# Kernel tuning notes

Hardware: AMD Instinct MI355X
Metric: run time of the kernel (lower is better)

The kernel has to match this reference:

```python
import jax, jax.numpy as jnp
import numpy as np

N = 100000
E = 1600000
IN_DIM = 165
HID = 128
OUT_H = 64  # hidden_dim // 2

def setup_inputs() -> dict:
    key = jax.random.key(0)
    ks = jax.random.split(key, 8)
    x = jax.random.normal(ks[0], (N, IN_DIM), dtype=jnp.float32)
    edge_index = jax.random.randint(ks[1], (2, E), 0, N, dtype=jnp.int64)
    s1 = 1.0 / np.sqrt(IN_DIM)
    s2 = 1.0 / np.sqrt(HID)
    s3 = 1.0 / np.sqrt(OUT_H)
    return {
        "x": x,
        "edge_index": edge_index,
        "W1": jax.random.normal(ks[2], (IN_DIM, HID), dtype=jnp.float32) * s1,
        "b1": jnp.zeros((HID,), jnp.float32),
        "Wg": jax.random.normal(ks[3], (HID, OUT_H), dtype=jnp.float32) * s2,
        "a_src": jax.random.normal(ks[4], (OUT_H,), dtype=jnp.float32) * s3,
        "a_dst": jax.random.normal(ks[5], (OUT_H,), dtype=jnp.float32) * s3,
        "bg": jnp.zeros((OUT_H,), jnp.float32),
        "Wfc": jax.random.normal(ks[6], (OUT_H, 2), dtype=jnp.float32) * s3,
        "bfc": jnp.zeros((2,), jnp.float32),
    }

def _add_self_loops(edge_index, n):
    loops = jnp.arange(n, dtype=edge_index.dtype)
    row = jnp.concatenate([edge_index[0], loops])
    col = jnpp_concat = jnp.concatenate([edge_index[1], loops])
    return row, col

def _gcn_layer(x, row, col, W, b, n):
    deg = jax.ops.segment_sum(jnp.ones_like(col, dtype=x.dtype), col, num_segments=n)
    dinv = jnp.where(deg > 0, jax.lax.rsqrt(deg), 0.0)
    h = x @ W                                   # [N, HID]
    msg = h[row] * (dinv[row] * dinv[col])[:, None]  # [E+N, HID]
    return jax.ops.segment_sum(msg, col, num_segments=n) + b

def _gat_layer(x, row, col, W, a_src, a_dst, b, n):
    # single-head GATConv with self-loops, LeakyReLU(0.2), segment softmax over dst
    h = x @ W                                   # [N, OUT_H]
    e = jax.nn.leaky_relu((h @ a_src)[row] + (h @ a_dst)[col], negative_slope=0.2)
    m = jax.ops.segment_max(e, col, num_segments=n)
    ex = jnp.exp(e - m[col])
    s = jax.ops.segment_sum(ex, col, num_segments=n)
    alpha = ex / s[col]                         # every node has a self-loop => s > 0
    out = jax.ops.segment_sum(alpha[:, None] * h[row], col, num_segments=n)
    return out + b

def reference(x, edge_index, W1, b1, Wg, a_src, a_dst, bg, Wfc, bfc):
    n = x.shape[0]
    row, col = _add_self_loops(edge_index, n)
    h = jax.nn.relu(_gcn_layer(x, row, col, W1, b1, n))
    h = jax.nn.relu(_gat_layer(h, row, col, Wg, a_src, a_dst, bg, n))
    return h @ Wfc + bfc
```

## Files before the change

### kernel.cpp

```cpp
#include <hip/hip_runtime.h>
#include <math.h>

#define NSL 0.2f
#define IN_DIM 165
#define HID 128
#define OUT_H 64
#define NCB_MAX 512
#define EPB 4096

typedef __attribute__((ext_vector_type(8))) short bf16x8;
typedef __attribute__((ext_vector_type(4))) float f32x4;

__device__ inline unsigned pack_bf16(float a, float b) {
    unsigned ua = __float_as_uint(a);
    ua += 0x7FFFu + ((ua >> 16) & 1u);
    unsigned ub = __float_as_uint(b);
    ub += 0x7FFFu + ((ub >> 16) & 1u);
    return (ua >> 16) | (ub & 0xFFFF0000u);
}

__device__ __host__ inline int pcol(int i) {
    int j = i >> 1, odd = i & 1;
    return 32 * (j >> 4) + (j & 15) + 16 * odd;
}

__global__ __launch_bounds__(256) void chist(const int* __restrict__ coli, int E,
                                             int* __restrict__ ghist, int ncb) {
    __shared__ int h[NCB_MAX];
    for (int i = threadIdx.x; i < ncb; i += 256) h[i] = 0;
    __syncthreads();
    int e0 = blockIdx.x * EPB;
    int e1 = min(e0 + EPB, E);
    for (int e = e0 + threadIdx.x; e < e1; e += 256)
        atomicAdd(&h[coli[e] >> 8], 1);
    __syncthreads();
    for (int i = threadIdx.x; i < ncb; i += 256)
        if (h[i]) atomicAdd(&ghist[i], h[i]);
}

__global__ __launch_bounds__(NCB_MAX) void cscan(const int* __restrict__ ghist,
                                                 int* __restrict__ cstart,
                                                 int* __restrict__ gcursor,
                                                 int ncb, int E) {
    __shared__ int tmp[NCB_MAX];
    int tid = threadIdx.x;
    int v = (tid < ncb) ? ghist[tid] : 0;
    tmp[tid] = v;
    __syncthreads();
    for (int off = 1; off < NCB_MAX; off <<= 1) {
        int t = (tid >= off) ? tmp[tid - off] : 0;
        __syncthreads();
        tmp[tid] += t;
        __syncthreads();
    }
    if (tid < ncb) {
        int excl = tmp[tid] - v;
        cstart[tid] = excl;
        gcursor[tid] = excl;
    }
    if (tid == ncb - 1) cstart[ncb] = E;
}

__global__ __launch_bounds__(256) void pass1_scatter(const int* __restrict__ rowi,
                                                     const int* __restrict__ coli, int E,
                                                     int* __restrict__ gcursor,
                                                     unsigned* __restrict__ ebuf, int ncb) {
    __shared__ int hist[NCB_MAX];
    __shared__ int base[NCB_MAX];
    int e0 = blockIdx.x * EPB;
    int e1 = min(e0 + EPB, E);
    for (int i = threadIdx.x; i < ncb; i += 256) hist[i] = 0;
    __syncthreads();
    for (int e = e0 + threadIdx.x; e < e1; e += 256)
        atomicAdd(&hist[coli[e] >> 8], 1);
    __syncthreads();
    for (int i = threadIdx.x; i < ncb; i += 256) {
        int h = hist[i];
        base[i] = h ? atomicAdd(&gcursor[i], h) : 0;
        hist[i] = 0;
    }
    __syncthreads();
    for (int e = e0 + threadIdx.x; e < e1; e += 256) {
        int c = coli[e];
        int cb = c >> 8;
        int rank = atomicAdd(&hist[cb], 1);
        ebuf[base[cb] + rank] = ((unsigned)rowi[e] << 8) | (unsigned)(c & 255);
    }
}

__global__ __launch_bounds__(256) void pass2_all(const unsigned* __restrict__ ebuf,
                                                 const int* __restrict__ cstart,
                                                 int* __restrict__ offsets,
                                                 float* __restrict__ dinv,
                                                 int* __restrict__ csr_src,
                                                 int n, int E) {
    __shared__ int cnt[256];
    __shared__ int scan[256];
    __shared__ int offs[256];
    const int tid = threadIdx.x;
    const int cb = blockIdx.x;
    cnt[tid] = 0;
    __syncthreads();
    int s = cstart[cb], e1 = cstart[cb + 1];
    for (int e = s + tid; e < e1; e += 256)
        atomicAdd(&cnt[ebuf[e] & 255u], 1);
    __syncthreads();
    int v = cnt[tid];
    scan[tid] = v;
    __syncthreads();
#pragma unroll
    for (int off = 1; off < 256; off <<= 1) {
        int t = (tid >= off) ? scan[tid - off] : 0;
        __syncthreads();
        scan[tid] += t;
        __syncthreads();
    }
    int off0 = s + scan[tid] - v;
    offs[tid] = off0;
    int node = (cb << 8) + tid;
    if (node < n) {
        offsets[node] = off0;
        dinv[node] = rsqrtf((float)v + 1.0f);
    }
    if (cb == 0 && tid == 0) offsets[n] = E;
    cnt[tid] = 0;
    __syncthreads();
    for (int e = s + tid; e < e1; e += 256) {
        unsigned u = ebuf[e];
        int local = u & 255u;
        int rank = atomicAdd(&cnt[local], 1);
        csr_src[offs[local] + rank] = (int)(u >> 8);
    }
}

__global__ __launch_bounds__(256) void wprep_all(const float* __restrict__ W1,
                                                 const float* __restrict__ b1,
                                                 const float* __restrict__ Wg,
                                                 const float* __restrict__ bg,
                                                 const float* __restrict__ Wfc,
                                                 uint4* __restrict__ wfrag,
                                                 float* __restrict__ b1p,
                                                 uint4* __restrict__ wg2frag,
                                                 float* __restrict__ bgp,
                                                 float2* __restrict__ wfcp) {
    int idx = blockIdx.x * 256 + threadIdx.x;
    if (idx < 3072) {
        int q = idx & 3, n = (idx >> 2) & 127, c = idx >> 9;
        int k0 = c * 32 + q * 8;
        float f[8];
#pragma unroll
        for (int j = 0; j < 8; j++) {
            int k = k0 + j;
            f[j] = (k < IN_DIM) ? W1[k * 128 + n] : 0.f;
        }
        uint4 u;
        u.x = pack_bf16(f[0], f[1]);
        u.y = pack_bf16(f[2], f[3]);
        u.z = pack_bf16(f[4], f[5]);
        u.w = pack_bf16(f[6], f[7]);
        wfrag[idx] = u;
    } else if (idx < 4096) {
        int i2 = idx - 3072;
        int q = i2 & 3, n = (i2 >> 2) & 63, c = i2 >> 8;
        float f[8];
#pragma unroll
        for (int j = 0; j < 8; j++) {
            int ks = c * 32 + q * 8 + j;
            f[j] = Wg[pcol(ks) * 64 + n];
        }
        uint4 u;
        u.x = pack_bf16(f[0], f[1]);
        u.y = pack_bf16(f[2], f[3]);
        u.z = pack_bf16(f[4], f[5]);
        u.w = pack_bf16(f[6], f[7]);
        wg2frag[i2] = u;
    }
    if (idx < 128) b1p[idx] = b1[pcol(idx)];
    if (idx < 64) {
        int o = pcol(idx);
        bgp[idx] = bg[o];
        wfcp[idx] = make_float2(Wfc[o * 2], Wfc[o * 2 + 1]);
    }
}

__global__ __launch_bounds__(256) void gemm1_mfma(const float* __restrict__ x,
                                                  const uint4* __restrict__ wfrag,
                                                  const float* __restrict__ dinv,
                                                  unsigned* __restrict__ h1p, int M) {
    const int t = threadIdx.x;
    const int wave = t >> 6;
    const int lane = t & 63;
    const int l16 = lane & 15;
    const int quad = lane >> 4;
    const int rowbase = blockIdx.x * 64 + wave * 16;

    int arow = rowbase + l16;
    if (arow >= M) arow = M - 1;
    const float* xr = x + (size_t)arow * IN_DIM;

    f32x4 acc[8];
#pragma unroll
    for (int nt = 0; nt < 8; nt++) acc[nt] = (f32x4){0.f, 0.f, 0.f, 0.f};

#pragma unroll
    for (int c = 0; c < 6; c++) {
        int k0 = c * 32 + quad * 8;
        float f[8];
#pragma unroll
        for (int j = 0; j < 8; j++)
            f[j] = (k0 + j < IN_DIM) ? xr[k0 + j] : 0.f;
        uint4 au;
        au.x = pack_bf16(f[0], f[1]);
        au.y = pack_bf16(f[2], f[3]);
        au.z = pack_bf16(f[4], f[5]);
        au.w = pack_bf16(f[6], f[7]);
        bf16x8 a = __builtin_bit_cast(bf16x8, au);
#pragma unroll
        for (int nt = 0; nt < 8; nt++) {
            uint4 bu = wfrag[(size_t)((c * 128 + nt * 16 + l16) * 4 + quad)];
            bf16x8 b = __builtin_bit_cast(bf16x8, bu);
            acc[nt] = __builtin_amdgcn_mfma_f32_16x16x32_bf16(a, b, acc[nt], 0, 0, 0);
        }
    }

#pragma unroll
    for (int r = 0; r < 4; r++) {
        int row = rowbase + quad * 4 + r;
        if (row < M) {
            float s = dinv[row];
#pragma unroll
            for (int p = 0; p < 4; p++) {
                h1p[(size_t)row * 64 + p * 16 + l16] =
                    pack_bf16(acc[2 * p][r] * s, acc[2 * p + 1][r] * s);
            }
        }
    }
}

__device__ inline void acc8(float* a, uint4 u) {
    a[0] += __uint_as_float(u.x << 16);
    a[1] += __uint_as_float(u.x & 0xFFFF0000u);
    a[2] += __uint_as_float(u.y << 16);
    a[3] += __uint_as_float(u.y & 0xFFFF0000u);
    a[4] += __uint_as_float(u.z << 16);
    a[5] += __uint_as_float(u.z & 0xFFFF0000u);
    a[6] += __uint_as_float(u.w << 16);
    a[7] += __uint_as_float(u.w & 0xFFFF0000u);
}

__device__ inline void fma8(float* a, uint4 u, float w) {
    a[0] = fmaf(__uint_as_float(u.x << 16), w, a[0]);
    a[1] = fmaf(__uint_as_float(u.x & 0xFFFF0000u), w, a[1]);
    a[2] = fmaf(__uint_as_float(u.y << 16), w, a[2]);
    a[3] = fmaf(__uint_as_float(u.y & 0xFFFF0000u), w, a[3]);
    a[4] = fmaf(__uint_as_float(u.z << 16), w, a[4]);
    a[5] = fmaf(__uint_as_float(u.z & 0xFFFF0000u), w, a[5]);
    a[6] = fmaf(__uint_as_float(u.w << 16), w, a[6]);
    a[7] = fmaf(__uint_as_float(u.w & 0xFFFF0000u), w, a[7]);
}

__device__ inline float lexp(float e) {
    e = e > 0.f ? e : NSL * e;
    return __expf(e);
}

__global__ __launch_bounds__(256) void gcn_gather(const int* __restrict__ offsets,
                                                  const int* __restrict__ csr_src,
                                                  const uint4* __restrict__ h1v,
                                                  const float* __restrict__ dinv,
                                                  const float* __restrict__ b1p,
                                                  uint4* __restrict__ gb, int n) {
    int node = (blockIdx.x * 256 + threadIdx.x) >> 4;
    int lane = threadIdx.x & 15;
    if (node >= n) return;
    int s0 = offsets[node], s1 = offsets[node + 1];

    float a0[8], a1[8], a2[8], a3[8];
#pragma unroll
    for (int i = 0; i < 8; i++) { a0[i] = 0.f; a1[i] = 0.f; a2[i] = 0.f; a3[i] = 0.f; }
    acc8(a0, h1v[(size_t)node * 16 + lane]);

    int k = s0;
    if (s1 - k >= 4) {
        int r0 = csr_src[k], r1 = csr_src[k + 1], r2 = csr_src[k + 2], r3 = csr_src[k + 3];
        uint4 v0 = h1v[(size_t)r0 * 16 + lane];
        uint4 v1 = h1v[(size_t)r1 * 16 + lane];
        uint4 v2 = h1v[(size_t)r2 * 16 + lane];
        uint4 v3 = h1v[(size_t)r3 * 16 + lane];
        k += 4;
        while (s1 - k >= 4) {
            int q0 = csr_src[k], q1 = csr_src[k + 1], q2 = csr_src[k + 2], q3 = csr_src[k + 3];
            uint4 u0 = h1v[(size_t)q0 * 16 + lane];
            uint4 u1 = h1v[(size_t)q1 * 16 + lane];
            uint4 u2 = h1v[(size_t)q2 * 16 + lane];
            uint4 u3 = h1v[(size_t)q3 * 16 + lane];
            k += 4;
            acc8(a0, v0);
            acc8(a1, v1);
            acc8(a2, v2);
            acc8(a3, v3);
            v0 = u0; v1 = u1; v2 = u2; v3 = u3;
        }
        acc8(a0, v0);
        acc8(a1, v1);
        acc8(a2, v2);
        acc8(a3, v3);
    }
    for (; k < s1; k++) {
        int r = csr_src[k];
        acc8(a0, h1v[(size_t)r * 16 + lane]);
    }

    float dc = dinv[node];
    float4 bb0 = ((const float4*)b1p)[lane * 2];
    float4 bb1 = ((const float4*)b1p)[lane * 2 + 1];
    float o[8];
    o[0] = fmaxf(((a0[0] + a1[0]) + (a2[0] + a3[0])) * dc + bb0.x, 0.f);
    o[1] = fmaxf(((a0[1] + a1[1]) + (a2[1] + a3[1])) * dc + bb0.y, 0.f);
    o[2] = fmaxf(((a0[2] + a1[2]) + (a2[2] + a3[2])) * dc + bb0.z, 0.f);
    o[3] = fmaxf(((a0[3] + a1[3]) + (a2[3] + a3[3])) * dc + bb0.w, 0.f);
    o[4] = fmaxf(((a0[4] + a1[4]) + (a2[4] + a3[4])) * dc + bb1.x, 0.f);
    o[5] = fmaxf(((a0[5] + a1[5]) + (a2[5] + a3[5])) * dc + bb1.y, 0.f);
    o[6] = fmaxf(((a0[6] + a1[6]) + (a2[6] + a3[6])) * dc + bb1.z, 0.f);
    o[7] = fmaxf(((a0[7] + a1[7]) + (a2[7] + a3[7])) * dc + bb1.w, 0.f);
    uint4 pk;
    pk.x = pack_bf16(o[0], o[1]);
    pk.y = pack_bf16(o[2], o[3]);
    pk.z = pack_bf16(o[4], o[5]);
    pk.w = pack_bf16(o[6], o[7]);
    gb[(size_t)node * 16 + lane] = pk;
}

__global__ __launch_bounds__(256) void gemm2_mfma(const uint4* __restrict__ gb4,
                                                  const uint4* __restrict__ wg2frag,
                                                  const float* __restrict__ a_src,
                                                  const float* __restrict__ a_dst,
                                                  unsigned* __restrict__ h2b,
                                                  float* __restrict__ es,
                                                  float* __restrict__ ed, int M) {
    const int t = threadIdx.x;
    const int wave = t >> 6;
    const int lane = t & 63;
    const int l16 = lane & 15;
    const int quad = lane >> 4;
    const int rowbase = blockIdx.x * 64 + wave * 16;

    int arow = rowbase + l16;
    if (arow >= M) arow = M - 1;

    f32x4 acc[4];
#pragma unroll
    for (int nt = 0; nt < 4; nt++) acc[nt] = (f32x4){0.f, 0.f, 0.f, 0.f};

#pragma unroll
    for (int c = 0; c < 4; c++) {
        uint4 au = gb4[(size_t)arow * 16 + c * 4 + quad];
        bf16x8 a = __builtin_bit_cast(bf16x8, au);
#pragma unroll
        for (int nt = 0; nt < 4; nt++) {
            uint4 bu = wg2frag[(size_t)((c * 64 + nt * 16 + l16) * 4 + quad)];
            bf16x8 b = __builtin_bit_cast(bf16x8, bu);
            acc[nt] = __builtin_amdgcn_mfma_f32_16x16x32_bf16(a, b, acc[nt], 0, 0, 0);
        }
    }

    float as0 = a_src[l16], as1 = a_src[16 + l16], as2 = a_src[32 + l16], as3 = a_src[48 + l16];
    float ad0 = a_dst[l16], ad1 = a_dst[16 + l16], ad2 = a_dst[32 + l16], ad3 = a_dst[48 + l16];

#pragma unroll
    for (int r = 0; r < 4; r++) {
        int row = rowbase + quad * 4 + r;
        float ps = acc[0][r] * as0 + acc[1][r] * as1 + acc[2][r] * as2 + acc[3][r] * as3;
        float pd = acc[0][r] * ad0 + acc[1][r] * ad1 + acc[2][r] * ad2 + acc[3][r] * ad3;
#pragma unroll
        for (int m = 8; m; m >>= 1) {
            ps += __shfl_xor(ps, m, 16);
            pd += __shfl_xor(pd, m, 16);
        }
        if (row < M) {
            h2b[(size_t)row * 32 + l16]      = pack_bf16(acc[0][r], acc[1][r]);
            h2b[(size_t)row * 32 + 16 + l16] = pack_bf16(acc[2][r], acc[3][r]);
            if (l16 == 0) { es[row] = ps; ed[row] = pd; }
        }
    }
}

__global__ __launch_bounds__(256) void gat_fused(const int* __restrict__ offsets,
                                                 const int* __restrict__ csr_src,
                                                 const uint4* __restrict__ h2v,
                                                 const float* __restrict__ es,
                                                 const float* __restrict__ ed,
                                                 const float* __restrict__ bgp,
                                                 const float2* __restrict__ wfcp,
                                                 const float* __restrict__ bfc,
                                                 float* __restrict__ out, int n) {
    int node = (blockIdx.x * 256 + threadIdx.x) >> 3;
    int lane = threadIdx.x & 7;
    if (node >= n) return;
    int s0 = offsets[node], s1 = offsets[node + 1];
    float edc = ed[node];

    float x0s = lexp(es[node] + edc);
    float sA = x0s, sB = 0.f, sC = 0.f, sD = 0.f;
    float aA[8], aB[8], aC[8], aD[8];
#pragma unroll
    for (int i = 0; i < 8; i++) { aA[i] = 0.f; aB[i] = 0.f; aC[i] = 0.f; aD[i] = 0.f; }
    fma8(aA, h2v[(size_t)node * 8 + lane], x0s);

    int k = s0;
    if (s1 - k >= 4) {
        int r0 = csr_src[k], r1 = csr_src[k + 1], r2 = csr_src[k + 2], r3 = csr_src[k + 3];
        float e0 = es[r0], e1 = es[r1], e2 = es[r2], e3 = es[r3];
        uint4 v0 = h2v[(size_t)r0 * 8 + lane];
        uint4 v1 = h2v[(size_t)r1 * 8 + lane];
        uint4 v2 = h2v[(size_t)r2 * 8 + lane];
        uint4 v3 = h2v[(size_t)r3 * 8 + lane];
        k += 4;
        while (s1 - k >= 4) {
            int q0 = csr_src[k], q1 = csr_src[k + 1], q2 = csr_src[k + 2], q3 = csr_src[k + 3];
            float f0 = es[q0], f1 = es[q1], f2 = es[q2], f3 = es[q3];
            uint4 u0 = h2v[(size_t)q0 * 8 + lane];
            uint4 u1 = h2v[(size_t)q1 * 8 + lane];
            uint4 u2 = h2v[(size_t)q2 * 8 + lane];
            uint4 u3 = h2v[(size_t)q3 * 8 + lane];
            k += 4;
            float x0 = lexp(e0 + edc), x1 = lexp(e1 + edc);
            float x2 = lexp(e2 + edc), x3 = lexp(e3 + edc);
            sA += x0; sB += x1; sC += x2; sD += x3;
            fma8(aA, v0, x0);
            fma8(aB, v1, x1);
            fma8(aC, v2, x2);
            fma8(aD, v3, x3);
            e0 = f0; e1 = f1; e2 = f2; e3 = f3;
            v0 = u0; v1 = u1; v2 = u2; v3 = u3;
        }
        float x0 = lexp(e0 + edc), x1 = lexp(e1 + edc);
        float x2 = lexp(e2 + edc), x3 = lexp(e3 + edc);
        sA += x0; sB += x1; sC += x2; sD += x3;
        fma8(aA, v0, x0);
        fma8(aB, v1, x1);
        fma8(aC, v2, x2);
        fma8(aD, v3, x3);
    }
    for (; k < s1; k++) {
        int r = csr_src[k];
        float xv = lexp(es[r] + edc);
        sA += xv;
        fma8(aA, h2v[(size_t)r * 8 + lane], xv);
    }
    float s = (sA + sB) + (sC + sD);
    float rcp = 1.0f / s;
    float4 b0 = ((const float4*)bgp)[lane * 2];
    float4 b1 = ((const float4*)bgp)[lane * 2 + 1];
    float o[8];
    o[0] = fmaxf(((aA[0] + aB[0]) + (aC[0] + aD[0])) * rcp + b0.x, 0.f);
    o[1] = fmaxf(((aA[1] + aB[1]) + (aC[1] + aD[1])) * rcp + b0.y, 0.f);
    o[2] = fmaxf(((aA[2] + aB[2]) + (aC[2] + aD[2])) * rcp + b0.z, 0.f);
    o[3] = fmaxf(((aA[3] + aB[3]) + (aC[3] + aD[3])) * rcp + b0.w, 0.f);
    o[4] = fmaxf(((aA[4] + aB[4]) + (aC[4] + aD[4])) * rcp + b1.x, 0.f);
    o[5] = fmaxf(((aA[5] + aB[5]) + (aC[5] + aD[5])) * rcp + b1.y, 0.f);
    o[6] = fmaxf(((aA[6] + aB[6]) + (aC[6] + aD[6])) * rcp + b1.z, 0.f);
    o[7] = fmaxf(((aA[7] + aB[7]) + (aC[7] + aD[7])) * rcp + b1.w, 0.f);

    float p0 = 0.f, p1 = 0.f;
#pragma unroll
    for (int m2 = 0; m2 < 4; m2++) {
        float4 w = ((const float4*)wfcp)[lane * 4 + m2];
        p0 += o[2 * m2] * w.x + o[2 * m2 + 1] * w.z;
        p1 += o[2 * m2] * w.y + o[2 * m2 + 1] * w.w;
    }
#pragma unroll
    for (int m = 4; m; m >>= 1) {
        p0 += __shfl_xor(p0, m, 8);
        p1 += __shfl_xor(p1, m, 8);
    }
    if (lane == 0) {
        out[(size_t)node * 2 + 0] = p0 + bfc[0];
        out[(size_t)node * 2 + 1] = p1 + bfc[1];
    }
}

extern "C" void kernel_launch(void* const* d_in, const int* in_sizes, int n_in,
                              void* d_out, int out_size, void* d_ws, size_t ws_size,
                              hipStream_t stream) {
    const float* x     = (const float*)d_in[0];
    const int*   ei    = (const int*)d_in[1];
    const float* W1    = (const float*)d_in[2];
    const float* b1    = (const float*)d_in[3];
    const float* Wg    = (const float*)d_in[4];
    const float* a_src = (const float*)d_in[5];
    const float* a_dst = (const float*)d_in[6];
    const float* bg    = (const float*)d_in[7];
    const float* Wfc   = (const float*)d_in[8];
    const float* bfc   = (const float*)d_in[9];
    float* out = (float*)d_out;

    const int N = in_sizes[0] / IN_DIM;
    const int E = in_sizes[1] / 2;
    const int* rowi = ei;
    const int* coli = ei + E;
    const int ncb = (N + 255) >> 8;

    auto alignup = [](char* p) { return (char*)(((uintptr_t)p + 15) & ~(uintptr_t)15); };

    char* wsb = (char*)d_ws;
    int*   offsets = (int*)wsb;
    float* dinv    = (float*)(offsets + N + 8);
    float* es      = dinv + N;
    float* ed      = es + N;
    int*   ghist   = (int*)(ed + N);
    int*   cstart  = ghist + NCB_MAX;
    int*   gcursor = cstart + NCB_MAX + 2;
    float* b1p     = (float*)(gcursor + NCB_MAX);
    float* bgp     = b1p + 128;
    float2* wfcp   = (float2*)(bgp + 64);
    uint4* wfrag   = (uint4*)alignup((char*)(wfcp + 64));
    uint4* wg2frag = wfrag + 3072;
    int*   csr_src = (int*)(wg2frag + 1024);
    unsigned* ebuf = (unsigned*)(csr_src + E);
    unsigned* h1p  = (unsigned*)alignup((char*)(ebuf + E));
    uint4* gb      = (uint4*)alignup((char*)(h1p + (size_t)N * 64));
    unsigned* h2b  = h1p;

    hipMemsetAsync(ghist, 0, NCB_MAX * 4, stream);

    const int nbE = (E + EPB - 1) / EPB;

    chist<<<nbE, 256, 0, stream>>>(coli, E, ghist, ncb);
    cscan<<<1, NCB_MAX, 0, stream>>>(ghist, cstart, gcursor, ncb, E);
    pass1_scatter<<<nbE, 256, 0, stream>>>(rowi, coli, E, gcursor, ebuf, ncb);
    pass2_all<<<ncb, 256, 0, stream>>>(ebuf, cstart, offsets, dinv, csr_src, N, E);

    wprep_all<<<16, 256, 0, stream>>>(W1, b1, Wg, bg, Wfc, wfrag, b1p, wg2frag, bgp, wfcp);

    gemm1_mfma<<<(N + 63) / 64, 256, 0, stream>>>(x, wfrag, dinv, h1p, N);

    gcn_gather<<<(N + 15) / 16, 256, 0, stream>>>(offsets, csr_src, (const uint4*)h1p,
                                                  dinv, b1p, gb, N);

    gemm2_mfma<<<(N + 63) / 64, 256, 0, stream>>>(gb, wg2frag, a_src, a_dst, h2b, es, ed, N);

    gat_fused<<<(N + 31) / 32, 256, 0, stream>>>(offsets, csr_src, (const uint4*)h2b,
                                                 es, ed, bgp, wfcp, bfc, out, N);
}
```

Measured before the change: 358.0 us.

## Quantize GCN hidden features to int8 with per-group bf16 scales for gather

The first GEMM now writes its scaled output as int8 values with one bf16 scale per 8-element group, instead of bf16. The GCN gather kernel reads 8 bytes of int8 plus a 2-byte scale per lane and dequantizes with FMAs. The goal is to shrink the bytes moved by the random-access neighbor gather, which is bandwidth bound, at the cost of lower numerical precision and a few extra ALU ops and shuffles.

```diff
diff --git a/kernel.cpp b/kernel.cpp
--- a/kernel.cpp
+++ b/kernel.cpp
@@ -186,7 +186,8 @@
 __global__ __launch_bounds__(256) void gemm1_mfma(const float* __restrict__ x,
                                                   const uint4* __restrict__ wfrag,
                                                   const float* __restrict__ dinv,
-                                                  unsigned* __restrict__ h1p, int M) {
+                                                  unsigned char* __restrict__ h1p8,
+                                                  unsigned short* __restrict__ scp, int M) {
     const int t = threadIdx.x;
     const int wave = t >> 6;
     const int lane = t & 63;
@@ -228,10 +229,21 @@
         int row = rowbase + quad * 4 + r;
         if (row < M) {
             float s = dinv[row];
+            unsigned short* hr = (unsigned short*)(h1p8 + (size_t)row * 128);
 #pragma unroll
             for (int p = 0; p < 4; p++) {
-                h1p[(size_t)row * 64 + p * 16 + l16] =
-                    pack_bf16(acc[2 * p][r] * s, acc[2 * p + 1][r] * s);
+                float v0 = acc[2 * p][r] * s;
+                float v1 = acc[2 * p + 1][r] * s;
+                float gm = fmaxf(fabsf(v0), fabsf(v1));
+                gm = fmaxf(gm, __shfl_xor(gm, 1));
+                gm = fmaxf(gm, __shfl_xor(gm, 2));
+                float inv = gm > 0.f ? 127.0f / gm : 0.f;
+                int q0 = (int)rintf(v0 * inv);
+                int q1 = (int)rintf(v1 * inv);
+                hr[p * 16 + l16] = (unsigned short)((q0 & 0xff) | ((q1 & 0xff) << 8));
+                if ((l16 & 3) == 0)
+                    scp[(size_t)row * 16 + 4 * p + (l16 >> 2)] =
+                        (unsigned short)(pack_bf16(gm * (1.0f / 127.0f), 0.f) & 0xffffu);
             }
         }
     }
@@ -248,6 +260,21 @@
     a[7] += __uint_as_float(u.w & 0xFFFF0000u);
 }
 
+__device__ inline void fma8i8(float* a, uint2 u, float s) {
+    a[0] = fmaf((float)(char)(u.x), s, a[0]);
+    a[1] = fmaf((float)(char)(u.x >> 8), s, a[1]);
+    a[2] = fmaf((float)(char)(u.x >> 16), s, a[2]);
+    a[3] = fmaf((float)(char)(u.x >> 24), s, a[3]);
+    a[4] = fmaf((float)(char)(u.y), s, a[4]);
+    a[5] = fmaf((float)(char)(u.y >> 8), s, a[5]);
+    a[6] = fmaf((float)(char)(u.y >> 16), s, a[6]);
+    a[7] = fmaf((float)(char)(u.y >> 24), s, a[7]);
+}
+
+__device__ inline float sdec(unsigned short sv) {
+    return __uint_as_float((unsigned)sv << 16);
+}
+
 __device__ inline void fma8(float* a, uint4 u, float w) {
     a[0] = fmaf(__uint_as_float(u.x << 16), w, a[0]);
     a[1] = fmaf(__uint_as_float(u.x & 0xFFFF0000u), w, a[1]);
@@ -266,7 +293,8 @@
 
 __global__ __launch_bounds__(256) void gcn_gather(const int* __restrict__ offsets,
                                                   const int* __restrict__ csr_src,
-                                                  const uint4* __restrict__ h1v,
+                                                  const uint2* __restrict__ h1v8,
+                                                  const unsigned short* __restrict__ scp,
                                                   const float* __restrict__ dinv,
                                                   const float* __restrict__ b1p,
                                                   uint4* __restrict__ gb, int n) {
@@ -278,37 +306,46 @@
     float a0[8], a1[8], a2[8], a3[8];
 #pragma unroll
     for (int i = 0; i < 8; i++) { a0[i] = 0.f; a1[i] = 0.f; a2[i] = 0.f; a3[i] = 0.f; }
-    acc8(a0, h1v[(size_t)node * 16 + lane]);
+    fma8i8(a0, h1v8[(size_t)node * 16 + lane], sdec(scp[(size_t)node * 16 + lane]));
 
     int k = s0;
     if (s1 - k >= 4) {
         int r0 = csr_src[k], r1 = csr_src[k + 1], r2 = csr_src[k + 2], r3 = csr_src[k + 3];
-        uint4 v0 = h1v[(size_t)r0 * 16 + lane];
-        uint4 v1 = h1v[(size_t)r1 * 16 + lane];
-        uint4 v2 = h1v[(size_t)r2 * 16 + lane];
-        uint4 v3 = h1v[(size_t)r3 * 16 + lane];
+        uint2 v0 = h1v8[(size_t)r0 * 16 + lane];
+        uint2 v1 = h1v8[(size_t)r1 * 16 + lane];
+        uint2 v2 = h1v8[(size_t)r2 * 16 + lane];
+        uint2 v3 = h1v8[(size_t)r3 * 16 + lane];
+        unsigned short w0 = scp[(size_t)r0 * 16 + lane];
+        unsigned short w1 = scp[(size_t)r1 * 16 + lane];
+        unsigned short w2 = scp[(size_t)r2 * 16 + lane];
+        unsigned short w3 = scp[(size_t)r3 * 16 + lane];
         k += 4;
         while (s1 - k >= 4) {
             int q0 = csr_src[k], q1 = csr_src[k + 1], q2 = csr_src[k + 2], q3 = csr_src[k + 3];
-            uint4 u0 = h1v[(size_t)q0 * 16 + lane];
-            uint4 u1 = h1v[(size_t)q1 * 16 + lane];
-            uint4 u2 = h1v[(size_t)q2 * 16 + lane];
-            uint4 u3 = h1v[(size_t)q3 * 16 + lane];
+            uint2 u0 = h1v8[(size_t)q0 * 16 + lane];
+            uint2 u1 = h1v8[(size_t)q1 * 16 + lane];
+            uint2 u2 = h1v8[(size_t)q2 * 16 + lane];
+            uint2 u3 = h1v8[(size_t)q3 * 16 + lane];
+            unsigned short y0 = scp[(size_t)q0 * 16 + lane];
+            unsigned short y1 = scp[(size_t)q1 * 16 + lane];
+            unsigned short y2 = scp[(size_t)q2 * 16 + lane];
+            unsigned short y3 = scp[(size_t)q3 * 16 + lane];
             k += 4;
-            acc8(a0, v0);
-            acc8(a1, v1);
-            acc8(a2, v2);
-            acc8(a3, v3);
+            fma8i8(a0, v0, sdec(w0));
+            fma8i8(a1, v1, sdec(w1));
+            fma8i8(a2, v2, sdec(w2));
+            fma8i8(a3, v3, sdec(w3));
             v0 = u0; v1 = u1; v2 = u2; v3 = u3;
-        }
-        acc8(a0, v0);
-        acc8(a1, v1);
-        acc8(a2, v2);
-        acc8(a3, v3);
+            w0 = y0; w1 = y1; w2 = y2; w3 = y3;
+        }
+        fma8i8(a0, v0, sdec(w0));
+        fma8i8(a1, v1, sdec(w1));
+        fma8i8(a2, v2, sdec(w2));
+        fma8i8(a3, v3, sdec(w3));
     }
     for (; k < s1; k++) {
         int r = csr_src[k];
-        acc8(a0, h1v[(size_t)r * 16 + lane]);
+        fma8i8(a0, h1v8[(size_t)r * 16 + lane], sdec(scp[(size_t)r * 16 + lane]));
     }
 
     float dc = dinv[node];
@@ -518,9 +555,10 @@
     uint4* wg2frag = wfrag + 3072;
     int*   csr_src = (int*)(wg2frag + 1024);
     unsigned* ebuf = (unsigned*)(csr_src + E);
-    unsigned* h1p  = (unsigned*)alignup((char*)(ebuf + E));
-    uint4* gb      = (uint4*)alignup((char*)(h1p + (size_t)N * 64));
-    unsigned* h2b  = h1p;
+    unsigned char* h1p8 = (unsigned char*)alignup((char*)(ebuf + E));
+    unsigned short* scp = (unsigned short*)(h1p8 + (size_t)N * 128);
+    uint4* gb      = (uint4*)alignup((char*)(scp + (size_t)N * 16));
+    unsigned* h2b  = (unsigned*)h1p8;
 
     hipMemsetAsync(ghist, 0, NCB_MAX * 4, stream);
 
@@ -533,10 +571,10 @@
 
     wprep_all<<<16, 256, 0, stream>>>(W1, b1, Wg, bg, Wfc, wfrag, b1p, wg2frag, bgp, wfcp);
 
-    gemm1_mfma<<<(N + 63) / 64, 256, 0, stream>>>(x, wfrag, dinv, h1p, N);
-
-    gcn_gather<<<(N + 15) / 16, 256, 0, stream>>>(offsets, csr_src, (const uint4*)h1p,
-                                                  dinv, b1p, gb, N);
+    gemm1_mfma<<<(N + 63) / 64, 256, 0, stream>>>(x, wfrag, dinv, h1p8, scp, N);
+
+    gcn_gather<<<(N + 15) / 16, 256, 0, stream>>>(offsets, csr_src, (const uint2*)h1p8,
+                                                  scp, dinv, b1p, gb, N);
 
     gemm2_mfma<<<(N + 63) / 64, 256, 0, stream>>>(gb, wg2frag, a_src, a_dst, h2b, es, ed, N);
 
```

Result: no change. 353.3 us (-1.3%).
